# Kernel optimization log

Hardware: AMD Instinct MI355X
Metric: run time of the kernel (lower is better)

## Reference

```python
import jax, jax.numpy as jnp
import numpy as np

N_TOKENS = 32768
NUM_EMB = 8192
EMB_DIM = 512
COMMITMENT_COST = 0.25


def setup_inputs() -> dict:
    key = jax.random.key(0)
    k1, k2 = jax.random.split(key)
    z_e = jax.random.normal(k1, (N_TOKENS, EMB_DIM), dtype=jnp.float32)
    codebook = jax.random.normal(k2, (NUM_EMB, EMB_DIM), dtype=jnp.float32)
    return {"z_e": z_e, "codebook": codebook}


def reference(z_e, codebook):
    # squared euclidean distances: [N, K]
    distances = (
        jnp.sum(z_e ** 2, axis=1, keepdims=True)
        + jnp.sum(codebook ** 2, axis=1)
        - 2.0 * z_e @ codebook.T
    )
    encoding_indices = jnp.argmin(distances, axis=1)  # [N]
    z_q = codebook[encoding_indices]  # [N, D]

    commitment_loss = jnp.mean((z_e - jax.lax.stop_gradient(z_q)) ** 2)
    vq_loss = COMMITMENT_COST * commitment_loss

    # straight-through estimator
    z_q_st = z_e + jax.lax.stop_gradient(z_q - z_e)
    return z_q_st, vq_loss, commitment_loss, encoding_indices
```

## Files before the change

### kernel.cpp

```cpp
#include <hip/hip_runtime.h>

#define N_TOKENS 32768
#define N_CODES  8192
#define DIM      512

#define BMT 128
#define BNT 128
#define SLICES 4
#define SLICE_CODES (N_CODES / SLICES)
#define NTILES (SLICE_CODES / BNT)
#define BK 32
#define CHUNKS (DIM / BK)
#define STEPS (NTILES * CHUNKS)

#define OUT_VQ     16777216
#define OUT_COMMIT 16777217
#define OUT_IDX    16777218

#define WS_CBHI 0
#define WS_CBLO 8388608
#define WS_NC   16777216
#define WS_PART 16809984
#define WS_ACC  17858560
#define WS_ZEHI 18874368
#define WS_ZELO 52428800
#define WS_NEED_FAST 85983232

typedef _Float16 f16x8 __attribute__((ext_vector_type(8)));
typedef _Float16 f16x4 __attribute__((ext_vector_type(4)));
typedef float    f32x4 __attribute__((ext_vector_type(4)));

__device__ __forceinline__ int sw32(int row, int kgrp) {
    return row * 32 + (((kgrp ^ ((row >> 1) & 3))) << 3);
}

__device__ __forceinline__ void async_copy16(void* lds, const void* g) {
    __builtin_amdgcn_global_load_lds(
        (const __attribute__((address_space(1))) unsigned int*)g,
        (__attribute__((address_space(3))) unsigned int*)lds,
        16, 0, 0);
}

__global__ void vq_prep_cb_kernel(const float* __restrict__ cb,
                                  _Float16* __restrict__ cb_hi,
                                  _Float16* __restrict__ cb_lo,
                                  float* __restrict__ nc,
                                  float* __restrict__ accum) {
    if (blockIdx.x == 0 && threadIdx.x == 0) *accum = 0.0f;
    const int wid  = threadIdx.x >> 6;
    const int lane = threadIdx.x & 63;
    const int row  = blockIdx.x * 4 + wid;
    const float4* src = (const float4*)(cb + (size_t)row * DIM);
    float4 v0 = src[lane * 2];
    float4 v1 = src[lane * 2 + 1];
    float s = v0.x*v0.x + v0.y*v0.y + v0.z*v0.z + v0.w*v0.w
            + v1.x*v1.x + v1.y*v1.y + v1.z*v1.z + v1.w*v1.w;
    f16x8 hi = {(_Float16)v0.x, (_Float16)v0.y, (_Float16)v0.z, (_Float16)v0.w,
                (_Float16)v1.x, (_Float16)v1.y, (_Float16)v1.z, (_Float16)v1.w};
    f16x8 lo = {(_Float16)(v0.x - (float)hi[0]), (_Float16)(v0.y - (float)hi[1]),
                (_Float16)(v0.z - (float)hi[2]), (_Float16)(v0.w - (float)hi[3]),
                (_Float16)(v1.x - (float)hi[4]), (_Float16)(v1.y - (float)hi[5]),
                (_Float16)(v1.z - (float)hi[6]), (_Float16)(v1.w - (float)hi[7])};
    *(f16x8*)&cb_hi[(size_t)row * DIM + lane * 8] = hi;
    *(f16x8*)&cb_lo[(size_t)row * DIM + lane * 8] = lo;
#pragma unroll
    for (int off = 32; off > 0; off >>= 1) s += __shfl_down(s, off);
    if (lane == 0) nc[row] = s;
}

__global__ void vq_prep_ze_kernel(const float* __restrict__ z_e,
                                  _Float16* __restrict__ ze_hi,
                                  _Float16* __restrict__ ze_lo) {
    const int wid  = threadIdx.x >> 6;
    const int lane = threadIdx.x & 63;
    const int row  = blockIdx.x * 4 + wid;
    const float4* src = (const float4*)(z_e + (size_t)row * DIM);
    float4 v0 = src[lane * 2];
    float4 v1 = src[lane * 2 + 1];
    f16x8 hi = {(_Float16)v0.x, (_Float16)v0.y, (_Float16)v0.z, (_Float16)v0.w,
                (_Float16)v1.x, (_Float16)v1.y, (_Float16)v1.z, (_Float16)v1.w};
    f16x8 lo = {(_Float16)(v0.x - (float)hi[0]), (_Float16)(v0.y - (float)hi[1]),
                (_Float16)(v0.z - (float)hi[2]), (_Float16)(v0.w - (float)hi[3]),
                (_Float16)(v1.x - (float)hi[4]), (_Float16)(v1.y - (float)hi[5]),
                (_Float16)(v1.z - (float)hi[6]), (_Float16)(v1.w - (float)hi[7])};
    *(f16x8*)&ze_hi[(size_t)row * DIM + lane * 8] = hi;
    *(f16x8*)&ze_lo[(size_t)row * DIM + lane * 8] = lo;
}

template <bool PRESPLIT>
__global__ __launch_bounds__(256, 2)
void vq_main_kernel(const float* __restrict__ z_e,
                    const _Float16* __restrict__ ze_hi,
                    const _Float16* __restrict__ ze_lo,
                    const _Float16* __restrict__ cb_hi,
                    const _Float16* __restrict__ cb_lo,
                    const float* __restrict__ nc,
                    float2* __restrict__ partials) {
    __shared__ __align__(16) unsigned char smem[65536];

    const int tid    = threadIdx.x;
    const int wid    = tid >> 6;
    const int lane   = tid & 63;
    const int wave_m = wid >> 1;
    const int wave_n = wid & 1;
    const int lane15 = lane & 15;
    const int quad   = lane >> 4;

    const int ns   = blockIdx.y;
    const int row0 = blockIdx.x * BMT;
    const int c00  = ns * SLICE_CODES;

    int aoff[4], boff[4];
#pragma unroll
    for (int i = 0; i < 4; ++i) {
        const int ra = wave_m * 64 + i * 16 + lane15;
        aoff[i] = sw32(ra, quad);
        const int rb = wave_n * 64 + i * 16 + lane15;
        boff[i] = sw32(rb, quad);
    }

    const int r4 = lane >> 2;
    const int sl = lane & 3;
    const int s_r0 = tid >> 3;
    const int s_cg = tid & 7;

    auto stage = [&](int buf, int step) {
        const int nt = step >> 4;
        const int kc = step & 15;
        const int c0 = c00 + nt * BNT;
        _Float16* base = (_Float16*)(smem + buf * 32768);
#pragma unroll
        for (int i = 0; i < 2; ++i) {
            const int L   = wid * 2 + i;
            const int row = L * 16 + r4;
            const int g   = sl ^ ((row >> 1) & 3);
            const size_t kb = (size_t)(c0 + row) * DIM + kc * BK + g * 8;
            async_copy16(base + 8192  + L * 512, cb_hi + kb);
            async_copy16(base + 12288 + L * 512, cb_lo + kb);
            if constexpr (PRESPLIT) {
                const size_t ka = (size_t)(row0 + row) * DIM + kc * BK + g * 8;
                async_copy16(base +        L * 512, ze_hi + ka);
                async_copy16(base + 4096 + L * 512, ze_lo + ka);
            }
        }
        if constexpr (!PRESPLIT) {
            _Float16* Ah = base;
            _Float16* Al = base + 4096;
#pragma unroll
            for (int rr = 0; rr < 4; ++rr) {
                const int row = rr * 32 + s_r0;
                float4 v = *(const float4*)&z_e[(size_t)(row0 + row) * DIM + kc * BK + s_cg * 4];
                f16x4 hi = {(_Float16)v.x, (_Float16)v.y, (_Float16)v.z, (_Float16)v.w};
                f16x4 lo = {(_Float16)(v.x - (float)hi[0]), (_Float16)(v.y - (float)hi[1]),
                            (_Float16)(v.z - (float)hi[2]), (_Float16)(v.w - (float)hi[3])};
                const int a = sw32(row, s_cg >> 1) + ((s_cg & 1) << 2);
                *(f16x4*)&Ah[a] = hi;
                *(f16x4*)&Al[a] = lo;
            }
        }
    };

    float minv[4][4];
    int   mini[4][4];
#pragma unroll
    for (int mi = 0; mi < 4; ++mi)
#pragma unroll
        for (int r = 0; r < 4; ++r) { minv[mi][r] = __builtin_inff(); mini[mi][r] = 0; }

    f32x4 acc[4][4];
    int buf = 0;
    stage(0, 0);

#pragma unroll 1
    for (int step = 0; step < STEPS; ++step) {
        const int nt = step >> 4;
        const int kc = step & 15;
        if (kc == 0) {
#pragma unroll
            for (int mi = 0; mi < 4; ++mi)
#pragma unroll
                for (int ni = 0; ni < 4; ++ni) acc[mi][ni] = (f32x4){0.f, 0.f, 0.f, 0.f};
        }

        __syncthreads();

        if (step + 1 < STEPS) stage(buf ^ 1, step + 1);

        _Float16* base = (_Float16*)(smem + buf * 32768);
        f16x8 ah[4], al[4], bh[4], bl[4];
#pragma unroll
        for (int mi = 0; mi < 4; ++mi) {
            ah[mi] = *(const f16x8*)&base[aoff[mi]];
            al[mi] = *(const f16x8*)&base[4096 + aoff[mi]];
        }
#pragma unroll
        for (int ni = 0; ni < 4; ++ni) {
            bh[ni] = *(const f16x8*)&base[8192 + boff[ni]];
            bl[ni] = *(const f16x8*)&base[12288 + boff[ni]];
        }
#pragma unroll
        for (int mi = 0; mi < 4; ++mi)
#pragma unroll
            for (int ni = 0; ni < 4; ++ni)
                acc[mi][ni] = __builtin_amdgcn_mfma_f32_16x16x32_f16(ah[mi], bh[ni], acc[mi][ni], 0, 0, 0);
#pragma unroll
        for (int mi = 0; mi < 4; ++mi)
#pragma unroll
            for (int ni = 0; ni < 4; ++ni)
                acc[mi][ni] = __builtin_amdgcn_mfma_f32_16x16x32_f16(al[mi], bh[ni], acc[mi][ni], 0, 0, 0);
#pragma unroll
        for (int mi = 0; mi < 4; ++mi)
#pragma unroll
            for (int ni = 0; ni < 4; ++ni)
                acc[mi][ni] = __builtin_amdgcn_mfma_f32_16x16x32_f16(ah[mi], bl[ni], acc[mi][ni], 0, 0, 0);

        if (kc == 15) {
            const int c0 = c00 + nt * BNT;
#pragma unroll
            for (int ni = 0; ni < 4; ++ni) {
                const int c = c0 + wave_n * 64 + ni * 16 + lane15;
                const float nrm = nc[c];
#pragma unroll
                for (int mi = 0; mi < 4; ++mi)
#pragma unroll
                    for (int r = 0; r < 4; ++r) {
                        const float v = fmaf(-2.0f, acc[mi][ni][r], nrm);
                        if (v < minv[mi][r]) { minv[mi][r] = v; mini[mi][r] = c; }
                    }
            }
        }
        buf ^= 1;
    }

    __syncthreads();
    float* redv = (float*)smem;
    int*   redi = (int*)(smem + 16384);
#pragma unroll
    for (int mi = 0; mi < 4; ++mi)
#pragma unroll
        for (int r = 0; r < 4; ++r) {
            const int rl = wave_m * 64 + mi * 16 + quad * 4 + r;
            const int o = wave_n * 2048 + rl * 16 + lane15;
            redv[o] = minv[mi][r];
            redi[o] = mini[mi][r];
        }
    __syncthreads();
    if (tid < BMT) {
        float bv = __builtin_inff();
        int   bi = 0x7fffffff;
        for (int j = 0; j < 32; ++j) {
            const int o = (j >= 16 ? 2048 : 0) + tid * 16 + (j & 15);
            const float v = redv[o];
            const int   i = redi[o];
            if (v < bv || (v == bv && i < bi)) { bv = v; bi = i; }
        }
        partials[(size_t)(row0 + tid) * SLICES + ns] = make_float2(bv, __int_as_float(bi));
    }
}

__global__ void vq_merge_kernel(const float* __restrict__ z_e,
                                const float* __restrict__ cb,
                                const float2* __restrict__ partials,
                                float* __restrict__ out,
                                float* __restrict__ accum) {
    __shared__ float wpart[4];
    const int wid  = threadIdx.x >> 6;
    const int lane = threadIdx.x & 63;
    const int tbase = blockIdx.x * 64 + wid * 16;
    float part = 0.0f;
#pragma unroll 1
    for (int t = 0; t < 16; ++t) {
        const int token = tbase + t;
        float bv = __builtin_inff();
        int   bi = 0;
#pragma unroll
        for (int s = 0; s < SLICES; ++s) {
            float2 p = partials[(size_t)token * SLICES + s];
            if (p.x < bv) { bv = p.x; bi = __float_as_int(p.y); }
        }
        const int code = bi & (N_CODES - 1);
        const float4* zp = (const float4*)(z_e + (size_t)token * DIM);
        const float4* cp = (const float4*)(cb + (size_t)code * DIM);
        float4* op = (float4*)out + (size_t)token * (DIM / 4);
#pragma unroll
        for (int i = 0; i < 2; ++i) {
            const int e = lane + i * 64;
            float4 z = zp[e];
            float4 q = cp[e];
            op[e] = q;
            float dx = z.x - q.x, dy = z.y - q.y, dz = z.z - q.z, dw = z.w - q.w;
            part += dx * dx + dy * dy + dz * dz + dw * dw;
        }
        if (lane == 0) out[OUT_IDX + token] = (float)code;
    }
#pragma unroll
    for (int off = 32; off > 0; off >>= 1) part += __shfl_down(part, off);
    if (lane == 0) wpart[wid] = part;
    __syncthreads();
    if (threadIdx.x == 0) atomicAdd(accum, wpart[0] + wpart[1] + wpart[2] + wpart[3]);
}

__global__ void vq_finalize_kernel(const float* __restrict__ accum,
                                   float* __restrict__ out) {
    const float c = *accum * (1.0f / (float)(N_TOKENS * DIM));
    out[OUT_VQ]     = 0.25f * c;
    out[OUT_COMMIT] = c;
}

extern "C" void kernel_launch(void* const* d_in, const int* in_sizes, int n_in,
                              void* d_out, int out_size, void* d_ws, size_t ws_size,
                              hipStream_t stream) {
    const float* z_e = (const float*)d_in[0];
    const float* cb  = (const float*)d_in[1];
    float* out = (float*)d_out;

    _Float16* cb_hi = (_Float16*)((char*)d_ws + WS_CBHI);
    _Float16* cb_lo = (_Float16*)((char*)d_ws + WS_CBLO);
    float*    nc    = (float*)((char*)d_ws + WS_NC);
    float2*   part  = (float2*)((char*)d_ws + WS_PART);
    float*    accum = (float*)((char*)d_ws + WS_ACC);
    _Float16* ze_hi = (_Float16*)((char*)d_ws + WS_ZEHI);
    _Float16* ze_lo = (_Float16*)((char*)d_ws + WS_ZELO);

    const bool fast = (ws_size >= (size_t)WS_NEED_FAST);

    hipLaunchKernelGGL(vq_prep_cb_kernel, dim3(N_CODES / 4), dim3(256), 0, stream,
                       cb, cb_hi, cb_lo, nc, accum);
    if (fast) {
        hipLaunchKernelGGL(vq_prep_ze_kernel, dim3(N_TOKENS / 4), dim3(256), 0, stream,
                           z_e, ze_hi, ze_lo);
        hipLaunchKernelGGL((vq_main_kernel<true>), dim3(N_TOKENS / BMT, SLICES), dim3(256), 0, stream,
                           z_e, ze_hi, ze_lo, cb_hi, cb_lo, nc, part);
    } else {
        hipLaunchKernelGGL((vq_main_kernel<false>), dim3(N_TOKENS / BMT, SLICES), dim3(256), 0, stream,
                           z_e, ze_hi, ze_lo, cb_hi, cb_lo, nc, part);
    }
    hipLaunchKernelGGL(vq_merge_kernel, dim3(N_TOKENS / 64), dim3(256), 0, stream,
                       z_e, cb, part, out, accum);
    hipLaunchKernelGGL(vq_finalize_kernel, dim3(1), dim3(1), 0, stream, accum, out);
}
```

Before: 905.6 us.

## Widen code tile to 256 and drop double-buffered LDS staging

Widens the code tile per block from 128 to 256, so each wave computes a 64x128 output block with 32 accumulators. That raises operand reuse from LDS and halves how often the A tile is restaged per code. The two-buffer async pipeline is replaced by one buffer with a sync-stage-sync pattern. This cuts LDS to 48KB but exposes load latency with no overlap. Doubling the accumulators raises register pressure, which may spill or lower occupancy under launch_bounds(256,2).

New measurement: 942.0 us. 4.0% more time.

```diff
diff --git a/kernel.cpp b/kernel.cpp
--- a/kernel.cpp
+++ b/kernel.cpp
@@ -5,13 +5,12 @@
 #define DIM      512
 
 #define BMT 128
-#define BNT 128
+#define BNT 256
 #define SLICES 4
 #define SLICE_CODES (N_CODES / SLICES)
 #define NTILES (SLICE_CODES / BNT)
 #define BK 32
 #define CHUNKS (DIM / BK)
-#define STEPS (NTILES * CHUNKS)
 
 #define OUT_VQ     16777216
 #define OUT_COMMIT 16777217
@@ -96,7 +95,11 @@
                     const _Float16* __restrict__ cb_lo,
                     const float* __restrict__ nc,
                     float2* __restrict__ partials) {
-    __shared__ __align__(16) unsigned char smem[65536];
+    __shared__ __align__(16) unsigned char smem[49152];
+    _Float16* As_hi = (_Float16*)smem;
+    _Float16* As_lo = (_Float16*)smem + 4096;
+    _Float16* Bs_hi = (_Float16*)smem + 8192;
+    _Float16* Bs_lo = (_Float16*)smem + 16384;
 
     const int tid    = threadIdx.x;
     const int wid    = tid >> 6;
@@ -110,42 +113,41 @@
     const int row0 = blockIdx.x * BMT;
     const int c00  = ns * SLICE_CODES;
 
-    int aoff[4], boff[4];
-#pragma unroll
-    for (int i = 0; i < 4; ++i) {
-        const int ra = wave_m * 64 + i * 16 + lane15;
-        aoff[i] = sw32(ra, quad);
-        const int rb = wave_n * 64 + i * 16 + lane15;
-        boff[i] = sw32(rb, quad);
-    }
+    int aoff[4], boff[8];
+#pragma unroll
+    for (int i = 0; i < 4; ++i)
+        aoff[i] = sw32(wave_m * 64 + i * 16 + lane15, quad);
+#pragma unroll
+    for (int i = 0; i < 8; ++i)
+        boff[i] = sw32(wave_n * 128 + i * 16 + lane15, quad);
 
     const int r4 = lane >> 2;
     const int sl = lane & 3;
     const int s_r0 = tid >> 3;
     const int s_cg = tid & 7;
 
-    auto stage = [&](int buf, int step) {
-        const int nt = step >> 4;
-        const int kc = step & 15;
+    auto stage = [&](int nt, int kc) {
         const int c0 = c00 + nt * BNT;
-        _Float16* base = (_Float16*)(smem + buf * 32768);
-#pragma unroll
-        for (int i = 0; i < 2; ++i) {
-            const int L   = wid * 2 + i;
+#pragma unroll
+        for (int i = 0; i < 4; ++i) {
+            const int L   = wid * 4 + i;
             const int row = L * 16 + r4;
             const int g   = sl ^ ((row >> 1) & 3);
             const size_t kb = (size_t)(c0 + row) * DIM + kc * BK + g * 8;
-            async_copy16(base + 8192  + L * 512, cb_hi + kb);
-            async_copy16(base + 12288 + L * 512, cb_lo + kb);
-            if constexpr (PRESPLIT) {
+            async_copy16(Bs_hi + L * 512, cb_hi + kb);
+            async_copy16(Bs_lo + L * 512, cb_lo + kb);
+        }
+        if constexpr (PRESPLIT) {
+#pragma unroll
+            for (int i = 0; i < 2; ++i) {
+                const int L   = wid * 2 + i;
+                const int row = L * 16 + r4;
+                const int g   = sl ^ ((row >> 1) & 3);
                 const size_t ka = (size_t)(row0 + row) * DIM + kc * BK + g * 8;
-                async_copy16(base +        L * 512, ze_hi + ka);
-                async_copy16(base + 4096 + L * 512, ze_lo + ka);
+                async_copy16(As_hi + L * 512, ze_hi + ka);
+                async_copy16(As_lo + L * 512, ze_lo + ka);
             }
-        }
-        if constexpr (!PRESPLIT) {
-            _Float16* Ah = base;
-            _Float16* Al = base + 4096;
+        } else {
 #pragma unroll
             for (int rr = 0; rr < 4; ++rr) {
                 const int row = rr * 32 + s_r0;
@@ -154,8 +156,8 @@
                 f16x4 lo = {(_Float16)(v.x - (float)hi[0]), (_Float16)(v.y - (float)hi[1]),
                             (_Float16)(v.z - (float)hi[2]), (_Float16)(v.w - (float)hi[3])};
                 const int a = sw32(row, s_cg >> 1) + ((s_cg & 1) << 2);
-                *(f16x4*)&Ah[a] = hi;
-                *(f16x4*)&Al[a] = lo;
+                *(f16x4*)&As_hi[a] = hi;
+                *(f16x4*)&As_lo[a] = lo;
             }
         }
     };
@@ -167,69 +169,68 @@
 #pragma unroll
         for (int r = 0; r < 4; ++r) { minv[mi][r] = __builtin_inff(); mini[mi][r] = 0; }
 
-    f32x4 acc[4][4];
-    int buf = 0;
-    stage(0, 0);
-
 #pragma unroll 1
-    for (int step = 0; step < STEPS; ++step) {
-        const int nt = step >> 4;
-        const int kc = step & 15;
-        if (kc == 0) {
+    for (int nt = 0; nt < NTILES; ++nt) {
+        const int c0 = c00 + nt * BNT;
+        f32x4 acc[4][8];
+#pragma unroll
+        for (int mi = 0; mi < 4; ++mi)
+#pragma unroll
+            for (int ni = 0; ni < 8; ++ni) acc[mi][ni] = (f32x4){0.f, 0.f, 0.f, 0.f};
+
+#pragma unroll 1
+        for (int kc = 0; kc < CHUNKS; ++kc) {
+            __syncthreads();
+            stage(nt, kc);
+            __syncthreads();
+
+            f16x8 ah[4], al[4];
+#pragma unroll
+            for (int mi = 0; mi < 4; ++mi) {
+                ah[mi] = *(const f16x8*)&As_hi[aoff[mi]];
+                al[mi] = *(const f16x8*)&As_lo[aoff[mi]];
+            }
+#pragma unroll
+            for (int nh = 0; nh < 2; ++nh) {
+                f16x8 bh[4], bl[4];
+#pragma unroll
+                for (int nj = 0; nj < 4; ++nj) {
+                    bh[nj] = *(const f16x8*)&Bs_hi[boff[nh * 4 + nj]];
+                    bl[nj] = *(const f16x8*)&Bs_lo[boff[nh * 4 + nj]];
+                }
+#pragma unroll
+                for (int mi = 0; mi < 4; ++mi)
+#pragma unroll
+                    for (int nj = 0; nj < 4; ++nj)
+                        acc[mi][nh * 4 + nj] = __builtin_amdgcn_mfma_f32_16x16x32_f16(
+                            ah[mi], bh[nj], acc[mi][nh * 4 + nj], 0, 0, 0);
+#pragma unroll
+                for (int mi = 0; mi < 4; ++mi)
+#pragma unroll
+                    for (int nj = 0; nj < 4; ++nj)
+                        acc[mi][nh * 4 + nj] = __builtin_amdgcn_mfma_f32_16x16x32_f16(
+                            al[mi], bh[nj], acc[mi][nh * 4 + nj], 0, 0, 0);
+#pragma unroll
+                for (int mi = 0; mi < 4; ++mi)
+#pragma unroll
+                    for (int nj = 0; nj < 4; ++nj)
+                        acc[mi][nh * 4 + nj] = __builtin_amdgcn_mfma_f32_16x16x32_f16(
+                            ah[mi], bl[nj], acc[mi][nh * 4 + nj], 0, 0, 0);
+            }
+        }
+
+#pragma unroll
+        for (int ni = 0; ni < 8; ++ni) {
+            const int c = c0 + wave_n * 128 + ni * 16 + lane15;
+            const float nrm = nc[c];
 #pragma unroll
             for (int mi = 0; mi < 4; ++mi)
 #pragma unroll
-                for (int ni = 0; ni < 4; ++ni) acc[mi][ni] = (f32x4){0.f, 0.f, 0.f, 0.f};
-        }
-
-        __syncthreads();
-
-        if (step + 1 < STEPS) stage(buf ^ 1, step + 1);
-
-        _Float16* base = (_Float16*)(smem + buf * 32768);
-        f16x8 ah[4], al[4], bh[4], bl[4];
-#pragma unroll
-        for (int mi = 0; mi < 4; ++mi) {
-            ah[mi] = *(const f16x8*)&base[aoff[mi]];
-            al[mi] = *(const f16x8*)&base[4096 + aoff[mi]];
-        }
-#pragma unroll
-        for (int ni = 0; ni < 4; ++ni) {
-            bh[ni] = *(const f16x8*)&base[8192 + boff[ni]];
-            bl[ni] = *(const f16x8*)&base[12288 + boff[ni]];
-        }
-#pragma unroll
-        for (int mi = 0; mi < 4; ++mi)
-#pragma unroll
-            for (int ni = 0; ni < 4; ++ni)
-                acc[mi][ni] = __builtin_amdgcn_mfma_f32_16x16x32_f16(ah[mi], bh[ni], acc[mi][ni], 0, 0, 0);
-#pragma unroll
-        for (int mi = 0; mi < 4; ++mi)
-#pragma unroll
-            for (int ni = 0; ni < 4; ++ni)
-                acc[mi][ni] = __builtin_amdgcn_mfma_f32_16x16x32_f16(al[mi], bh[ni], acc[mi][ni], 0, 0, 0);
-#pragma unroll
-        for (int mi = 0; mi < 4; ++mi)
-#pragma unroll
-            for (int ni = 0; ni < 4; ++ni)
-                acc[mi][ni] = __builtin_amdgcn_mfma_f32_16x16x32_f16(ah[mi], bl[ni], acc[mi][ni], 0, 0, 0);
-
-        if (kc == 15) {
-            const int c0 = c00 + nt * BNT;
-#pragma unroll
-            for (int ni = 0; ni < 4; ++ni) {
-                const int c = c0 + wave_n * 64 + ni * 16 + lane15;
-                const float nrm = nc[c];
-#pragma unroll
-                for (int mi = 0; mi < 4; ++mi)
-#pragma unroll
-                    for (int r = 0; r < 4; ++r) {
-                        const float v = fmaf(-2.0f, acc[mi][ni][r], nrm);
-                        if (v < minv[mi][r]) { minv[mi][r] = v; mini[mi][r] = c; }
-                    }
-            }
-        }
-        buf ^= 1;
+                for (int r = 0; r < 4; ++r) {
+                    const float v = fmaf(-2.0f, acc[mi][ni][r], nrm);
+                    if (v < minv[mi][r]) { minv[mi][r] = v; mini[mi][r] = c; }
+                }
+        }
     }
 
     __syncthreads();
```
